# Performance work log

Hardware: AMD Instinct MI355X
Metric: run time of the kernel (lower is better)

## Reference

```python
import jax, jax.numpy as jnp
import numpy as np

TAU = 0.08


def setup_inputs() -> dict:
    key = jax.random.key(0)
    k1, k2 = jax.random.split(key)
    pos_waves = jax.random.normal(k1, (32, 64, 8192), dtype=jnp.float32)
    neg_waves = jax.random.normal(k2, (32, 64, 8192), dtype=jnp.float32)
    return {"pos_waves": pos_waves, "neg_waves": neg_waves}


def _normalize(w):
    # global min/max over the whole wave tensor (matches torch.min/torch.max on 2D tensor)
    lo = jnp.min(w, axis=(1, 2), keepdims=True)  # [N,1,1]
    hi = jnp.max(w, axis=(1, 2), keepdims=True)
    return (w - lo) / (hi - lo)


def _pairwise_negpearson(X, Y):
    # X: [N,B,T], Y: [M,B,T] -> mean over B of (1 - pearson) for every (n,m) pair
    T = X.shape[-1]
    sx = jnp.sum(X, axis=-1)            # [N,B]
    sy = jnp.sum(Y, axis=-1)            # [M,B]
    sx2 = jnp.sum(X * X, axis=-1)       # [N,B]
    sy2 = jnp.sum(Y * Y, axis=-1)       # [M,B]
    sxy = jnp.einsum('nbt,mbt->nmb', X, Y)  # [N,M,B]
    num = T * sxy - sx[:, None, :] * sy[None, :, :]
    den = jnp.sqrt((T * sx2 - sx * sx)[:, None, :] * (T * sy2 - sy * sy)[None, :, :])
    return jnp.mean(1.0 - num / den, axis=-1)  # [N,M]


def reference(pos_waves, neg_waves):
    P = _normalize(pos_waves)   # [N,B,T]
    Q = _normalize(neg_waves)   # [M,B,T]
    N = P.shape[0]

    d_pp = _pairwise_negpearson(P, P)                    # [N,N]
    upper = jnp.triu(jnp.ones((N, N), dtype=bool), k=1)  # i < j pairs only
    pos_total = jnp.sum(jnp.where(upper, jnp.exp(d_pp / TAU), 0.0))

    d_pn = _pairwise_negpearson(P, Q)                    # [N,M]
    neg_total = jnp.sum(jnp.exp(d_pn / TAU))

    return jnp.log10(pos_total / neg_total + 1.0)
```

## Files before the change

kernel.cpp:

```cpp
#include <hip/hip_runtime.h>
#include <cmath>

#define N_ 32
#define B_ 64
#define T_ 8192
#define CPB 16
#define PSTRIDE 2176
#define PADH 264

typedef _Float16 half4 __attribute__((ext_vector_type(4)));
typedef _Float16 half8 __attribute__((ext_vector_type(8)));
typedef float floatx4 __attribute__((ext_vector_type(4)));

__global__ __launch_bounds__(512, 8) void k_stage1(const float* __restrict__ pos,
                                                   const float* __restrict__ neg,
                                                   float* __restrict__ partial) {
    __shared__ _Float16 tile[2][32][PADH];

    const int bid = blockIdx.x;
    const int b = bid >> 4, c = bid & 15;
    const int tid = threadIdx.x;
    const int wave = tid >> 6, lane = tid & 63;
    const int row = tid >> 4;
    const int idx = tid & 15;
    const int mat = wave >> 2;
    const int qi = (wave >> 1) & 1, qj = wave & 1;
    const int m16 = lane & 15, h2 = lane >> 4;

    const float* xrow = pos + ((long)row * B_ + b) * T_ + c * 512;
    const float* yrow = neg + ((long)row * B_ + b) * T_ + c * 512;

    floatx4 acc = {};
    float sx = 0.f, sx2 = 0.f, sy = 0.f, sy2 = 0.f;

#pragma unroll
    for (int s = 0; s < 2; ++s) {
        __syncthreads();
        const float4* px = (const float4*)(xrow + s * 256);
        const float4* py = (const float4*)(yrow + s * 256);

        float4 vx[4], vy[4];
#pragma unroll
        for (int f = 0; f < 4; ++f) vx[f] = px[f * 16 + idx];
#pragma unroll
        for (int f = 0; f < 4; ++f) vy[f] = py[f * 16 + idx];
#pragma unroll
        for (int f = 0; f < 4; ++f) {
            float4 v = vx[f];
            sx += v.x + v.y + v.z + v.w;
            sx2 = fmaf(v.x, v.x, sx2); sx2 = fmaf(v.y, v.y, sx2);
            sx2 = fmaf(v.z, v.z, sx2); sx2 = fmaf(v.w, v.w, sx2);
            half4 hv = {(_Float16)v.x, (_Float16)v.y, (_Float16)v.z, (_Float16)v.w};
            *(half4*)&tile[0][row][(f * 16 + idx) * 4] = hv;
        }
#pragma unroll
        for (int f = 0; f < 4; ++f) {
            float4 u = vy[f];
            sy += u.x + u.y + u.z + u.w;
            sy2 = fmaf(u.x, u.x, sy2); sy2 = fmaf(u.y, u.y, sy2);
            sy2 = fmaf(u.z, u.z, sy2); sy2 = fmaf(u.w, u.w, sy2);
            half4 hu = {(_Float16)u.x, (_Float16)u.y, (_Float16)u.z, (_Float16)u.w};
            *(half4*)&tile[1][row][(f * 16 + idx) * 4] = hu;
        }
        __syncthreads();

        const _Float16* abase = &tile[0][qi * 16 + m16][h2 * 8];
        const _Float16* bbase = &tile[mat][qj * 16 + m16][h2 * 8];
#pragma unroll
        for (int k = 0; k < 8; ++k) {
            half8 af = *(const half8*)(abase + k * 32);
            half8 bf = *(const half8*)(bbase + k * 32);
            acc = __builtin_amdgcn_mfma_f32_16x16x32_f16(af, bf, acc, 0, 0, 0);
        }
    }

    sx += __shfl_xor(sx, 1); sx += __shfl_xor(sx, 2);
    sx += __shfl_xor(sx, 4); sx += __shfl_xor(sx, 8);
    sx2 += __shfl_xor(sx2, 1); sx2 += __shfl_xor(sx2, 2);
    sx2 += __shfl_xor(sx2, 4); sx2 += __shfl_xor(sx2, 8);
    sy += __shfl_xor(sy, 1); sy += __shfl_xor(sy, 2);
    sy += __shfl_xor(sy, 4); sy += __shfl_xor(sy, 8);
    sy2 += __shfl_xor(sy2, 1); sy2 += __shfl_xor(sy2, 2);
    sy2 += __shfl_xor(sy2, 4); sy2 += __shfl_xor(sy2, 8);

    float* out = partial + (long)bid * PSTRIDE;
    if ((tid & 15) < 4) {
        int kind = tid & 3;
        float v = (kind == 0) ? sx : (kind == 1) ? sx2 : (kind == 2) ? sy : sy2;
        out[2048 + kind * 32 + row] = v;
    }

#pragma unroll
    for (int reg = 0; reg < 4; ++reg) {
        int rr = qi * 16 + h2 * 4 + reg;
        int cc = qj * 16 + m16;
        out[mat * 1024 + rr * 32 + cc] = acc[reg];
    }
}

__global__ void k_reduce(const float* __restrict__ partial, float* __restrict__ red) {
    const int b = blockIdx.y;
    const int o = blockIdx.x * 128 + threadIdx.x;
    const float* in = partial + (long)b * CPB * PSTRIDE;
    float s = 0.f;
#pragma unroll
    for (int c = 0; c < CPB; ++c) s += in[c * PSTRIDE + o];
    red[(long)b * PSTRIDE + o] = s;
}

__global__ void k_entries(const float* __restrict__ red, double* __restrict__ blocksums) {
    const int tid = threadIdx.x;
    const int w = tid >> 6, lane = tid & 63;
    const int entry = blockIdx.x * 4 + w;
    const int mat = entry >> 10;
    const int idx = entry & 1023;
    const int n = idx >> 5, m = idx & 31;

    const float* rb = red + (long)lane * PSTRIDE;
    float g = rb[mat * 1024 + idx];
    float sxn = rb[2048 + n];
    float sx2n = rb[2080 + n];
    float sym, sy2m;
    if (mat == 0) {
        sym = rb[2048 + m];
        sy2m = rb[2080 + m];
    } else {
        sym = rb[2112 + m];
        sy2m = rb[2144 + m];
    }

    double num = (double)T_ * (double)g - (double)sxn * (double)sym;
    double vx = (double)T_ * (double)sx2n - (double)sxn * (double)sxn;
    double vy = (double)T_ * (double)sy2m - (double)sym * (double)sym;
    double contrib = 1.0 - num / sqrt(vx * vy);

#pragma unroll
    for (int off = 32; off; off >>= 1) contrib += __shfl_down(contrib, off);

    __shared__ double s_pos[4], s_neg[4];
    if (lane == 0) {
        double d = contrib * (1.0 / B_);
        double term = exp(d / 0.08);
        double p = 0.0, q = 0.0;
        if (mat == 0) {
            if (n < m) p = term;
        } else {
            q = term;
        }
        s_pos[w] = p;
        s_neg[w] = q;
    }
    __syncthreads();
    if (tid == 0) {
        blocksums[blockIdx.x * 2 + 0] = s_pos[0] + s_pos[1] + s_pos[2] + s_pos[3];
        blocksums[blockIdx.x * 2 + 1] = s_neg[0] + s_neg[1] + s_neg[2] + s_neg[3];
    }
}

__global__ void k_final(const double* __restrict__ blocksums, float* __restrict__ out) {
    __shared__ double sp[256], sn[256];
    const int tid = threadIdx.x;
    double p = 0.0, q = 0.0;
    for (int i = tid; i < 512; i += 256) {
        p += blocksums[2 * i + 0];
        q += blocksums[2 * i + 1];
    }
    sp[tid] = p;
    sn[tid] = q;
    __syncthreads();
    for (int s = 128; s; s >>= 1) {
        if (tid < s) {
            sp[tid] += sp[tid + s];
            sn[tid] += sn[tid + s];
        }
        __syncthreads();
    }
    if (tid == 0) out[0] = (float)log10(sp[0] / sn[0] + 1.0);
}

extern "C" void kernel_launch(void* const* d_in, const int* in_sizes, int n_in,
                              void* d_out, int out_size, void* d_ws, size_t ws_size,
                              hipStream_t stream) {
    const float* pos = (const float*)d_in[0];
    const float* neg = (const float*)d_in[1];
    float* out = (float*)d_out;

    char* ws = (char*)d_ws;
    float* partial = (float*)ws;
    float* red = (float*)(ws + (size_t)1024 * PSTRIDE * 4);
    double* blocksums = (double*)(ws + (size_t)1024 * PSTRIDE * 4 + (size_t)64 * PSTRIDE * 4);

    k_stage1<<<1024, 512, 0, stream>>>(pos, neg, partial);
    k_reduce<<<dim3(17, 64), 128, 0, stream>>>(partial, red);
    k_entries<<<512, 256, 0, stream>>>(red, blocksums);
    k_final<<<1, 256, 0, stream>>>(blocksums, out);
}
```

Baseline: 154.1 us.

## Load tiles directly into LDS via global_load_lds and convert to fp16 on read

Replaces register-staged global loads plus fp16 conversion and LDS stores with direct global-to-LDS async loads (global_load_lds) of fp32 data, in four chunks of 128 elements. The fp32-to-fp16 conversion moves to the MFMA operand read, and row sums and sums of squares are computed from LDS by a separate thread mapping. The goal is to cut VGPR traffic and the store instructions in the load path. In exchange, LDS footprint doubles because it holds fp32, each chunk waits on vmcnt(0) with no overlap, and every value is converted once per wave that reads it.

```diff
diff --git a/kernel.cpp b/kernel.cpp
--- a/kernel.cpp
+++ b/kernel.cpp
@@ -6,89 +6,90 @@
 #define T_ 8192
 #define CPB 16
 #define PSTRIDE 2176
-#define PADH 264
+#define PAIRF 260
+#define TENSF 4160
+#define LDSB  33280
 
-typedef _Float16 half4 __attribute__((ext_vector_type(4)));
 typedef _Float16 half8 __attribute__((ext_vector_type(8)));
 typedef float floatx4 __attribute__((ext_vector_type(4)));
 
 __global__ __launch_bounds__(512, 8) void k_stage1(const float* __restrict__ pos,
                                                    const float* __restrict__ neg,
                                                    float* __restrict__ partial) {
-    __shared__ _Float16 tile[2][32][PADH];
+    __shared__ __align__(16) float smem[LDSB / 4];
 
     const int bid = blockIdx.x;
     const int b = bid >> 4, c = bid & 15;
     const int tid = threadIdx.x;
     const int wave = tid >> 6, lane = tid & 63;
-    const int row = tid >> 4;
-    const int idx = tid & 15;
-    const int mat = wave >> 2;
-    const int qi = (wave >> 1) & 1, qj = wave & 1;
+
+    const int tzw = wave >> 2;
+    const int quad = wave & 3;
+    const float* gsrc = tzw ? neg : pos;
+    const float* gptr[4];
+    int ldsoff[4];
+#pragma unroll
+    for (int j = 0; j < 4; ++j) {
+        int p = quad * 4 + j;
+        int row = 2 * p + (lane >> 5);
+        gptr[j] = gsrc + ((long)(row * B_ + b)) * T_ + c * 512 + (lane & 31) * 4;
+        ldsoff[j] = tzw * TENSF + p * PAIRF;
+    }
+
+    const int mat = wave >> 2, qi = (wave >> 1) & 1, qj = wave & 1;
     const int m16 = lane & 15, h2 = lane >> 4;
+    const int arow = qi * 16 + m16, brow = qj * 16 + m16;
+    const float* aptr = smem + ((arow >> 1) * PAIRF + (arow & 1) * 128);
+    const float* bptr = smem + mat * TENSF + ((brow >> 1) * PAIRF + (brow & 1) * 128);
 
-    const float* xrow = pos + ((long)row * B_ + b) * T_ + c * 512;
-    const float* yrow = neg + ((long)row * B_ + b) * T_ + c * 512;
+    const int stream = tid >> 3, sub = tid & 7;
+    const int srow = stream & 31, stz = stream >> 5;
+    const float* sptr = smem + stz * TENSF + ((srow >> 1) * PAIRF + (srow & 1) * 128) + sub * 16;
 
     floatx4 acc = {};
-    float sx = 0.f, sx2 = 0.f, sy = 0.f, sy2 = 0.f;
+    float ssum = 0.f, ssq = 0.f;
+
+    for (int ch = 0; ch < 4; ++ch) {
+#pragma unroll
+        for (int j = 0; j < 4; ++j) {
+            __builtin_amdgcn_global_load_lds(
+                (const __attribute__((address_space(1))) void*)(gptr[j] + ch * 128),
+                (__attribute__((address_space(3))) void*)(smem + ldsoff[j]), 16, 0, 0);
+        }
+        asm volatile("s_waitcnt vmcnt(0)" ::: "memory");
+        __syncthreads();
 
 #pragma unroll
-    for (int s = 0; s < 2; ++s) {
-        __syncthreads();
-        const float4* px = (const float4*)(xrow + s * 256);
-        const float4* py = (const float4*)(yrow + s * 256);
+        for (int kk = 0; kk < 4; ++kk) {
+            const int t0 = kk * 32 + h2 * 8;
+            float4 a0 = *(const float4*)(aptr + t0);
+            float4 a1 = *(const float4*)(aptr + t0 + 4);
+            float4 b0 = *(const float4*)(bptr + t0);
+            float4 b1 = *(const float4*)(bptr + t0 + 4);
+            half8 af = {(_Float16)a0.x, (_Float16)a0.y, (_Float16)a0.z, (_Float16)a0.w,
+                        (_Float16)a1.x, (_Float16)a1.y, (_Float16)a1.z, (_Float16)a1.w};
+            half8 bf = {(_Float16)b0.x, (_Float16)b0.y, (_Float16)b0.z, (_Float16)b0.w,
+                        (_Float16)b1.x, (_Float16)b1.y, (_Float16)b1.z, (_Float16)b1.w};
+            acc = __builtin_amdgcn_mfma_f32_16x16x32_f16(af, bf, acc, 0, 0, 0);
+        }
 
-        float4 vx[4], vy[4];
-#pragma unroll
-        for (int f = 0; f < 4; ++f) vx[f] = px[f * 16 + idx];
-#pragma unroll
-        for (int f = 0; f < 4; ++f) vy[f] = py[f * 16 + idx];
 #pragma unroll
         for (int f = 0; f < 4; ++f) {
-            float4 v = vx[f];
-            sx += v.x + v.y + v.z + v.w;
-            sx2 = fmaf(v.x, v.x, sx2); sx2 = fmaf(v.y, v.y, sx2);
-            sx2 = fmaf(v.z, v.z, sx2); sx2 = fmaf(v.w, v.w, sx2);
-            half4 hv = {(_Float16)v.x, (_Float16)v.y, (_Float16)v.z, (_Float16)v.w};
-            *(half4*)&tile[0][row][(f * 16 + idx) * 4] = hv;
+            float4 v = *(const float4*)(sptr + f * 4);
+            ssum += v.x + v.y + v.z + v.w;
+            ssq = fmaf(v.x, v.x, ssq); ssq = fmaf(v.y, v.y, ssq);
+            ssq = fmaf(v.z, v.z, ssq); ssq = fmaf(v.w, v.w, ssq);
         }
-#pragma unroll
-        for (int f = 0; f < 4; ++f) {
-            float4 u = vy[f];
-            sy += u.x + u.y + u.z + u.w;
-            sy2 = fmaf(u.x, u.x, sy2); sy2 = fmaf(u.y, u.y, sy2);
-            sy2 = fmaf(u.z, u.z, sy2); sy2 = fmaf(u.w, u.w, sy2);
-            half4 hu = {(_Float16)u.x, (_Float16)u.y, (_Float16)u.z, (_Float16)u.w};
-            *(half4*)&tile[1][row][(f * 16 + idx) * 4] = hu;
-        }
+
         __syncthreads();
-
-        const _Float16* abase = &tile[0][qi * 16 + m16][h2 * 8];
-        const _Float16* bbase = &tile[mat][qj * 16 + m16][h2 * 8];
-#pragma unroll
-        for (int k = 0; k < 8; ++k) {
-            half8 af = *(const half8*)(abase + k * 32);
-            half8 bf = *(const half8*)(bbase + k * 32);
-            acc = __builtin_amdgcn_mfma_f32_16x16x32_f16(af, bf, acc, 0, 0, 0);
-        }
     }
 
-    sx += __shfl_xor(sx, 1); sx += __shfl_xor(sx, 2);
-    sx += __shfl_xor(sx, 4); sx += __shfl_xor(sx, 8);
-    sx2 += __shfl_xor(sx2, 1); sx2 += __shfl_xor(sx2, 2);
-    sx2 += __shfl_xor(sx2, 4); sx2 += __shfl_xor(sx2, 8);
-    sy += __shfl_xor(sy, 1); sy += __shfl_xor(sy, 2);
-    sy += __shfl_xor(sy, 4); sy += __shfl_xor(sy, 8);
-    sy2 += __shfl_xor(sy2, 1); sy2 += __shfl_xor(sy2, 2);
-    sy2 += __shfl_xor(sy2, 4); sy2 += __shfl_xor(sy2, 8);
+    ssum += __shfl_xor(ssum, 1); ssum += __shfl_xor(ssum, 2); ssum += __shfl_xor(ssum, 4);
+    ssq += __shfl_xor(ssq, 1); ssq += __shfl_xor(ssq, 2); ssq += __shfl_xor(ssq, 4);
 
     float* out = partial + (long)bid * PSTRIDE;
-    if ((tid & 15) < 4) {
-        int kind = tid & 3;
-        float v = (kind == 0) ? sx : (kind == 1) ? sx2 : (kind == 2) ? sy : sy2;
-        out[2048 + kind * 32 + row] = v;
-    }
+    if (sub == 0) out[2048 + (stz * 2 + 0) * 32 + srow] = ssum;
+    if (sub == 1) out[2048 + (stz * 2 + 1) * 32 + srow] = ssq;
 
 #pragma unroll
     for (int reg = 0; reg < 4; ++reg) {
```

Result: slower. 167.0 us (+8.4%).
